# Kernel optimization log

Measured on AMD Instinct MI355X. Metric: run time of the kernel, lower is better.

Reference implementation:

```python
import jax, jax.numpy as jnp
import numpy as np

EPS = 1e-5

def _bn(x, gamma, beta):
    # training-mode BatchNorm1d over (batch, length) per channel; x: [B, C, N]
    mean = x.mean(axis=(0, 2), keepdims=True)
    var = x.var(axis=(0, 2), keepdims=True)
    return (x - mean) * jax.lax.rsqrt(var + EPS) * gamma[None, :, None] + beta[None, :, None]

def setup_inputs() -> dict:
    key = jax.random.key(0)
    ks = jax.random.split(key, 16)
    B, N = 8, 4096
    def w(k, o, i):
        return jax.random.normal(k, (o, i), jnp.float32) * (1.0 / np.sqrt(i))
    return {
        "x": jax.random.normal(ks[0], (B, 3, N), jnp.float32),
        "w_mlp1": w(ks[1], 64, 3),
        "g1": jax.random.uniform(ks[2], (64,), jnp.float32, 0.5, 1.5),
        "b1": jax.random.normal(ks[3], (64,), jnp.float32) * 0.1,
        "w_mlp2": w(ks[4], 128, 64),
        "wq": w(ks[5], 16, 128),
        "g2": jax.random.uniform(ks[6], (16,), jnp.float32, 0.5, 1.5),
        "b2": jax.random.normal(ks[7], (16,), jnp.float32) * 0.1,
        "wk": w(ks[8], 16, 128),
        "g3": jax.random.uniform(ks[9], (16,), jnp.float32, 0.5, 1.5),
        "b3": jax.random.normal(ks[10], (16,), jnp.float32) * 0.1,
        "wv": w(ks[11], 3, 128),
        "g4": jax.random.uniform(ks[12], (3,), jnp.float32, 0.5, 1.5),
        "b4": jax.random.normal(ks[13], (3,), jnp.float32) * 0.1,
        "alpha": jax.random.uniform(ks[14], (1,), jnp.float32, 0.1, 1.0),
    }

def reference(x, w_mlp1, g1, b1, w_mlp2, wq, g2, b2, wk, g3, b3, wv, g4, b4, alpha):
    # mlp: conv1(k=1) -> BN -> LeakyReLU(0.2) -> conv1(k=1)
    h = jnp.einsum('oc,bcn->bon', w_mlp1, x)                       # [B,64,N]
    h = jax.nn.leaky_relu(_bn(h, g1, b1), negative_slope=0.2)
    feat = jnp.einsum('oc,bcn->bon', w_mlp2, h)                    # [B,128,N]
    q = jax.nn.relu(_bn(jnp.einsum('oc,bcn->bon', wq, feat), g2, b2))  # [B,16,N]
    k = jax.nn.relu(_bn(jnp.einsum('oc,bcn->bon', wk, feat), g3, b3))  # [B,16,N]
    v = jax.nn.relu(_bn(jnp.einsum('oc,bcn->bon', wv, feat), g4, b4))  # [B,3,N]
    # similarity = softmax(K^T Q) over last dim (no scale, as in source)
    sim = jax.nn.softmax(jnp.einsum('bdn,bdm->bnm', k, q), axis=-1)    # [B,N,N]
    # out = V @ sim^T
    out = jnp.einsum('bcm,bnm->bcn', v, sim)                           # [B,3,N]
    return alpha[0] * out + x
```

## Files before the change

kernel.cpp:

```cpp
#include <hip/hip_runtime.h>

#define EPS 1e-5f
constexpr int NN = 4096;
constexpr float INV_CNT = 1.0f / (8.0f * 4096.0f);
constexpr float LOG2E = 1.44269504f;

typedef __attribute__((ext_vector_type(8))) short bf16x8;
typedef __attribute__((ext_vector_type(4))) float f32x4;
typedef __attribute__((ext_vector_type(16))) float f32x16;
typedef __attribute__((ext_vector_type(4))) _Float16 f16x4;
typedef __fp16 fp16x2 __attribute__((ext_vector_type(2)));

#if __has_builtin(__builtin_amdgcn_exp2f)
#define EXP2F(x) __builtin_amdgcn_exp2f(x)
#else
#define EXP2F(x) exp2f(x)
#endif

constexpr size_t OFF_QPT = 0;
constexpr size_t OFF_KPT = 524288;
constexpr size_t OFF_VPT = 1048576;
constexpr size_t OFF_WT2 = 1179648;
constexpr size_t OFF_XP  = 1181952;
constexpr size_t OFF_BS  = 1183104;
constexpr size_t OFF_QH  = 1201024;
constexpr size_t OFF_QL  = 1463168;
constexpr size_t OFF_KH  = 1725312;
constexpr size_t OFF_KL  = 1987456;
constexpr size_t OFF_VFH = 2249600;
constexpr size_t OFF_PL  = 2511744;
constexpr size_t OFF_PA0 = 2773888;
constexpr size_t OFF_PA1 = 3036032;
constexpr size_t OFF_PA2 = 3298176;
constexpr size_t OFF_PMX = 3560320;

__global__ __launch_bounds__(256) void kA_mom_wcomb(
    const float* __restrict__ x, float* __restrict__ xpart,
    const float* __restrict__ w2, const float* __restrict__ wq,
    const float* __restrict__ wk, const float* __restrict__ wv,
    float* __restrict__ wt2) {
  __shared__ float w2s[8192];
  __shared__ float wr[4480];
  __shared__ float sred[36];
  int tx = threadIdx.x;
  if (blockIdx.x < 128) {
    int idx = blockIdx.x * 256 + tx;
    int b = idx >> 12, n = idx & 4095;
    float x0 = x[(size_t)(b*3+0)*NN + n];
    float x1 = x[(size_t)(b*3+1)*NN + n];
    float x2 = x[(size_t)(b*3+2)*NN + n];
    float m[9] = {x0, x1, x2, x0*x0, x0*x1, x0*x2, x1*x1, x1*x2, x2*x2};
    #pragma unroll
    for (int off = 32; off; off >>= 1) {
      #pragma unroll
      for (int j = 0; j < 9; ++j) m[j] += __shfl_xor(m[j], off);
    }
    int w = tx >> 6;
    if ((tx & 63) == 0) {
      #pragma unroll
      for (int j = 0; j < 9; ++j) sred[w*9+j] = m[j];
    }
    __syncthreads();
    if (tx < 9) xpart[tx*128 + blockIdx.x] = sred[tx] + sred[9+tx] + sred[18+tx] + sred[27+tx];
  } else {
    for (int i = tx; i < 8192; i += 256) w2s[i] = w2[i];
    for (int i = tx; i < 2048; i += 256) { wr[i] = wq[i]; wr[2048+i] = wk[i]; }
    for (int i = tx; i < 384; i += 256) wr[4096+i] = wv[i];
    __syncthreads();
    for (int e = tx; e < 2240; e += 256) {
      int j = e >> 6, c = e & 63;
      float s = 0.f;
      #pragma unroll 4
      for (int o = 0; o < 128; ++o) s = fmaf(wr[j*128+o], w2s[o*64+c], s);
      wt2[c*36 + j] = s;
    }
  }
}

__global__ __launch_bounds__(128) void kB_qkv(
    const float* __restrict__ x, const float* __restrict__ xpart,
    const float* __restrict__ w1, const float* __restrict__ g1,
    const float* __restrict__ b1, const float* __restrict__ wt2,
    float* __restrict__ qpT, float* __restrict__ kpT, float* __restrict__ vpT,
    float* __restrict__ bs) {
  __shared__ float4 w1s[64];
  __shared__ float4 wt2s[576];
  __shared__ float sred[140];
  __shared__ float mom[9];
  int tx = threadIdx.x;
  for (int i = tx; i < 576; i += 128) wt2s[i] = ((const float4*)wt2)[i];
  if (tx < 9) {
    float acc = 0.f;
    #pragma unroll 8
    for (int i = 0; i < 128; ++i) acc += xpart[tx*128 + i];
    mom[tx] = acc * INV_CNT;
  }
  __syncthreads();
  if (tx < 64) {
    int c = tx;
    float a = w1[c*3], b_ = w1[c*3+1], d = w1[c*3+2];
    float mean = a*mom[0] + b_*mom[1] + d*mom[2];
    float e2 = a*a*mom[3] + b_*b_*mom[6] + d*d*mom[8]
             + 2.f*(a*b_*mom[4] + a*d*mom[5] + b_*d*mom[7]);
    float sc = g1[c] * rsqrtf(e2 - mean*mean + EPS);
    w1s[c] = make_float4(a*sc, b_*sc, d*sc, fmaf(-mean, sc, b1[c]));
  }
  __syncthreads();
  int idx = blockIdx.x*128 + tx;
  int b = idx >> 12, n = idx & 4095;
  float x0 = x[(size_t)(b*3+0)*NN + n];
  float x1 = x[(size_t)(b*3+1)*NN + n];
  float x2 = x[(size_t)(b*3+2)*NN + n];
  float qa[16] = {}, ka[16] = {};
  float va0 = 0.f, va1 = 0.f, va2 = 0.f;
  #pragma unroll 4
  for (int c = 0; c < 64; ++c) {
    float4 w = w1s[c];
    float h = fmaf(w.x, x0, fmaf(w.y, x1, fmaf(w.z, x2, w.w)));
    h = h > 0.f ? h : 0.2f*h;
    #pragma unroll
    for (int j = 0; j < 4; ++j) {
      float4 A = wt2s[c*9 + j];
      qa[4*j+0] = fmaf(A.x, h, qa[4*j+0]);
      qa[4*j+1] = fmaf(A.y, h, qa[4*j+1]);
      qa[4*j+2] = fmaf(A.z, h, qa[4*j+2]);
      qa[4*j+3] = fmaf(A.w, h, qa[4*j+3]);
      float4 B = wt2s[c*9 + 4 + j];
      ka[4*j+0] = fmaf(B.x, h, ka[4*j+0]);
      ka[4*j+1] = fmaf(B.y, h, ka[4*j+1]);
      ka[4*j+2] = fmaf(B.z, h, ka[4*j+2]);
      ka[4*j+3] = fmaf(B.w, h, ka[4*j+3]);
    }
    float4 V = wt2s[c*9 + 8];
    va0 = fmaf(V.x, h, va0); va1 = fmaf(V.y, h, va1); va2 = fmaf(V.z, h, va2);
  }
  float4* qo = (float4*)(qpT + (size_t)idx*16);
  float4* ko = (float4*)(kpT + (size_t)idx*16);
  #pragma unroll
  for (int j = 0; j < 4; ++j) {
    qo[j] = make_float4(qa[4*j], qa[4*j+1], qa[4*j+2], qa[4*j+3]);
    ko[j] = make_float4(ka[4*j], ka[4*j+1], ka[4*j+2], ka[4*j+3]);
  }
  ((float4*)vpT)[idx] = make_float4(va0, va1, va2, 0.f);
  int w = tx >> 6;
  bool lead = ((tx & 63) == 0);
  #pragma unroll
  for (int d = 0; d < 16; ++d) {
    float s = qa[d], q = qa[d]*qa[d];
    #pragma unroll
    for (int off = 32; off; off >>= 1) { s += __shfl_xor(s, off); q += __shfl_xor(q, off); }
    if (lead) { sred[w*70 + d] = s; sred[w*70 + 16 + d] = q; }
    s = ka[d]; q = ka[d]*ka[d];
    #pragma unroll
    for (int off = 32; off; off >>= 1) { s += __shfl_xor(s, off); q += __shfl_xor(q, off); }
    if (lead) { sred[w*70 + 32 + d] = s; sred[w*70 + 48 + d] = q; }
  }
  float vv[3] = {va0, va1, va2};
  #pragma unroll
  for (int d = 0; d < 3; ++d) {
    float s = vv[d], q = vv[d]*vv[d];
    #pragma unroll
    for (int off = 32; off; off >>= 1) { s += __shfl_xor(s, off); q += __shfl_xor(q, off); }
    if (lead) { sred[w*70 + 64 + d] = s; sred[w*70 + 67 + d] = q; }
  }
  __syncthreads();
  if (tx < 70)
    bs[tx*256 + blockIdx.x] = sred[tx] + sred[70+tx];
}

__global__ __launch_bounds__(256) void kC_prep(
    const float* __restrict__ qpT, const float* __restrict__ kpT,
    const float* __restrict__ vpT, const float* __restrict__ bs,
    const float* __restrict__ g2, const float* __restrict__ b2,
    const float* __restrict__ g3, const float* __restrict__ b3,
    const float* __restrict__ g4, const float* __restrict__ b4,
    uint4* __restrict__ qh, uint4* __restrict__ ql,
    uint4* __restrict__ kh, uint4* __restrict__ kl,
    _Float16* __restrict__ vfh) {
  __shared__ float tot[70];
  __shared__ float spr[70];
  int tx = threadIdx.x;
  if (tx < 70) {
    float acc = 0.f;
    #pragma unroll 8
    for (int i = 0; i < 256; ++i) acc += bs[tx*256 + i];
    tot[tx] = acc * INV_CNT;
  }
  __syncthreads();
  if (tx < 16) {
    float mean = tot[tx], var = tot[16+tx] - mean*mean;
    float sc = g2[tx]*rsqrtf(var + EPS);
    spr[tx] = sc * LOG2E;
    spr[16+tx] = fmaf(-mean, sc, b2[tx]) * LOG2E;
  } else if (tx < 32) {
    int d = tx-16;
    float mean = tot[32+d], var = tot[48+d] - mean*mean;
    float sc = g3[d]*rsqrtf(var + EPS);
    spr[32+d] = sc; spr[48+d] = fmaf(-mean, sc, b3[d]);
  } else if (tx < 35) {
    int d = tx-32;
    float mean = tot[64+d], var = tot[67+d] - mean*mean;
    float sc = g4[d]*rsqrtf(var + EPS);
    spr[64+d] = sc; spr[67+d] = fmaf(-mean, sc, b4[d]);
  }
  __syncthreads();
  int p = blockIdx.x*256 + tx;
  float qv[16], kv[16];
  const float4* q4 = (const float4*)(qpT + (size_t)p*16);
  const float4* k4p = (const float4*)(kpT + (size_t)p*16);
  #pragma unroll
  for (int j = 0; j < 4; ++j) {
    float4 tq = q4[j], tk = k4p[j];
    qv[4*j] = tq.x; qv[4*j+1] = tq.y; qv[4*j+2] = tq.z; qv[4*j+3] = tq.w;
    kv[4*j] = tk.x; kv[4*j+1] = tk.y; kv[4*j+2] = tk.z; kv[4*j+3] = tk.w;
  }
  #pragma unroll
  for (int d = 0; d < 16; ++d) {
    qv[d] = fmaxf(fmaf(qv[d], spr[d],    spr[16+d]), 0.f);
    kv[d] = fmaxf(fmaf(kv[d], spr[32+d], spr[48+d]), 0.f);
  }
  unsigned qhw[8], qlw[8], khw[8], klw[8];
  #pragma unroll
  for (int j = 0; j < 8; ++j) {
    unsigned u0 = __float_as_uint(qv[2*j]),   u1 = __float_as_uint(qv[2*j+1]);
    unsigned h0 = u0 & 0xFFFF0000u, h1 = u1 & 0xFFFF0000u;
    float l0 = qv[2*j] - __uint_as_float(h0);
    float l1 = qv[2*j+1] - __uint_as_float(h1);
    qhw[j] = (h0 >> 16) | h1;
    qlw[j] = (__float_as_uint(l0) >> 16) | (__float_as_uint(l1) & 0xFFFF0000u);
    u0 = __float_as_uint(kv[2*j]); u1 = __float_as_uint(kv[2*j+1]);
    h0 = u0 & 0xFFFF0000u; h1 = u1 & 0xFFFF0000u;
    l0 = kv[2*j] - __uint_as_float(h0);
    l1 = kv[2*j+1] - __uint_as_float(h1);
    khw[j] = (h0 >> 16) | h1;
    klw[j] = (__float_as_uint(l0) >> 16) | (__float_as_uint(l1) & 0xFFFF0000u);
  }
  qh[(size_t)p*2+0] = make_uint4(qhw[0], qhw[1], qhw[2], qhw[3]);
  qh[(size_t)p*2+1] = make_uint4(qhw[4], qhw[5], qhw[6], qhw[7]);
  ql[(size_t)p*2+0] = make_uint4(qlw[0], qlw[1], qlw[2], qlw[3]);
  ql[(size_t)p*2+1] = make_uint4(qlw[4], qlw[5], qlw[6], qlw[7]);
  kh[(size_t)p*2+0] = make_uint4(khw[0], khw[1], khw[2], khw[3]);
  kh[(size_t)p*2+1] = make_uint4(khw[4], khw[5], khw[6], khw[7]);
  kl[(size_t)p*2+0] = make_uint4(klw[0], klw[1], klw[2], klw[3]);
  kl[(size_t)p*2+1] = make_uint4(klw[4], klw[5], klw[6], klw[7]);
  float4 vv = ((const float4*)vpT)[p];
  vfh[0*32768 + p] = (_Float16)fmaxf(fmaf(vv.x, spr[64], spr[67]), 0.f);
  vfh[1*32768 + p] = (_Float16)fmaxf(fmaf(vv.y, spr[65], spr[68]), 0.f);
  vfh[2*32768 + p] = (_Float16)fmaxf(fmaf(vv.z, spr[66], spr[69]), 0.f);
  vfh[3*32768 + p] = (_Float16)1.0f;
}

__global__ __launch_bounds__(256, 4) void k5max(
    const uint4* __restrict__ qh, const uint4* __restrict__ kh,
    float* __restrict__ pmax2) {
  int tx = threadIdx.x;
  int cc = blockIdx.x & 3;
  int rc = (blockIdx.x >> 2) & 31;
  int b  = blockIdx.x >> 7;
  int w = tx >> 6, lane = tx & 63;
  int cl = lane & 31, hl = lane >> 5;
  int n0 = rc*128 + w*32;
  size_t pbase = (size_t)b*4096;
  bf16x8 aK = *(const bf16x8*)&kh[(pbase + n0 + cl)*2 + hl];
  f32x16 zero16;
  #pragma unroll
  for (int r = 0; r < 16; ++r) zero16[r] = 0.f;
  f32x16 lm = zero16;
  const uint4* qptr = &qh[(pbase + (size_t)cc*1024 + cl)*2 + hl];
  bf16x8 bQ1 = *(const bf16x8*)qptr;
  bf16x8 bQ2 = *(const bf16x8*)(qptr + 64);
  #pragma unroll 2
  for (int ct = 0; ct < 16; ++ct) {
    bf16x8 q1 = bQ1, q2 = bQ2;
    qptr += 128;
    if (ct < 15) {
      bQ1 = *(const bf16x8*)qptr;
      bQ2 = *(const bf16x8*)(qptr + 64);
    }
    f32x16 c1 = __builtin_amdgcn_mfma_f32_32x32x16_bf16(aK, q1, zero16, 0, 0, 0);
    f32x16 c2 = __builtin_amdgcn_mfma_f32_32x32x16_bf16(aK, q2, zero16, 0, 0, 0);
    #pragma unroll
    for (int r = 0; r < 16; ++r)
      lm[r] = fmaxf(fmaxf(lm[r], c1[r]), c2[r]);
  }
  #pragma unroll
  for (int off = 1; off <= 16; off <<= 1) {
    #pragma unroll
    for (int r = 0; r < 16; ++r) lm[r] = fmaxf(lm[r], __shfl_xor(lm[r], off));
  }
  if (cl == 0) {
    #pragma unroll
    for (int r = 0; r < 16; ++r)
      pmax2[(size_t)cc*32768 + pbase + n0 + (r & 3) + 8*(r >> 2) + 4*hl] = lm[r];
  }
}

#define K5_TILE(BKH, BKL, MR, ACC)                                             \
  {                                                                            \
    f32x4 c = __builtin_amdgcn_mfma_f32_16x16x32_bf16(aQ, BKH, zero4, 0, 0, 0);\
    c = __builtin_amdgcn_mfma_f32_16x16x32_bf16(aQ, BKL, c, 0, 0, 0);          \
    union { fp16x2 h2[2]; f16x4 v4; } pw;                                      \
    pw.h2[0] = __builtin_amdgcn_cvt_pkrtz(EXP2F(c[0] - MR), EXP2F(c[1] - MR)); \
    pw.h2[1] = __builtin_amdgcn_cvt_pkrtz(EXP2F(c[2] - MR), EXP2F(c[3] - MR)); \
    ACC = __builtin_amdgcn_mfma_f32_16x16x16f16(av, pw.v4, ACC, 0, 0, 0);      \
  }

__global__ __launch_bounds__(128, 5) void k5pv(
    const uint4* __restrict__ qh, const uint4* __restrict__ ql,
    const uint4* __restrict__ kh, const uint4* __restrict__ kl,
    const _Float16* __restrict__ vfh, const float* __restrict__ pmax2,
    float* __restrict__ pl, float* __restrict__ pa0,
    float* __restrict__ pa1, float* __restrict__ pa2) {
  int tx = threadIdx.x;
  int cb = blockIdx.x & 7;
  int rb = blockIdx.x >> 3;
  int b  = rb >> 5;
  int rc = rb & 31;
  int w = tx >> 6, lane = tx & 63;
  int nl = lane & 15, g = lane >> 4, g1 = g & 1;
  int n0 = rc*128 + w*64;
  size_t pbase = (size_t)b*4096;
  size_t kp0 = (pbase + n0 + nl)*2 + g1;
  bf16x8 bKh0 = *(const bf16x8*)&kh[kp0];
  bf16x8 bKl0 = *(const bf16x8*)&kl[kp0];
  bf16x8 bKh1 = *(const bf16x8*)&kh[kp0 + 32];
  bf16x8 bKl1 = *(const bf16x8*)&kl[kp0 + 32];
  bf16x8 bKh2 = *(const bf16x8*)&kh[kp0 + 64];
  bf16x8 bKl2 = *(const bf16x8*)&kl[kp0 + 64];
  bf16x8 bKh3 = *(const bf16x8*)&kh[kp0 + 96];
  bf16x8 bKl3 = *(const bf16x8*)&kl[kp0 + 96];
  size_t mi = pbase + n0 + nl;
  float M0, M1, M2, M3;
  {
    float a0 = fmaxf(pmax2[mi],      pmax2[32768 + mi]);
    float b0 = fmaxf(pmax2[2*32768 + mi], pmax2[3*32768 + mi]);
    M0 = fmaxf(a0, b0);
    a0 = fmaxf(pmax2[mi+16],      pmax2[32768 + mi+16]);
    b0 = fmaxf(pmax2[2*32768 + mi+16], pmax2[3*32768 + mi+16]);
    M1 = fmaxf(a0, b0);
    a0 = fmaxf(pmax2[mi+32],      pmax2[32768 + mi+32]);
    b0 = fmaxf(pmax2[2*32768 + mi+32], pmax2[3*32768 + mi+32]);
    M2 = fmaxf(a0, b0);
    a0 = fmaxf(pmax2[mi+48],      pmax2[32768 + mi+48]);
    b0 = fmaxf(pmax2[2*32768 + mi+48], pmax2[3*32768 + mi+48]);
    M3 = fmaxf(a0, b0);
  }
  f32x4 zero4 = {0.f, 0.f, 0.f, 0.f};
  f32x4 acc0 = zero4, acc1 = zero4, acc2 = zero4, acc3 = zero4;
  size_t cbase = pbase + (size_t)cb*512;
  const uint4* qptr = ((g < 2) ? qh : ql) + (cbase + nl)*2 + g1;
  const _Float16* vptr = vfh + (size_t)nl*32768 + cbase + g*4;
  bool vload = (nl < 4);
  f16x4 zeroh = {(_Float16)0.f, (_Float16)0.f, (_Float16)0.f, (_Float16)0.f};
  bf16x8 aQn = *(const bf16x8*)qptr;
  f16x4 avn = zeroh;
  if (vload) avn = *(const f16x4*)vptr;
  #pragma unroll 2
  for (int ct = 0; ct < 32; ++ct) {
    bf16x8 aQ = aQn;
    f16x4 av = avn;
    qptr += 32;
    vptr += 16;
    if (ct < 31) {
      aQn = *(const bf16x8*)qptr;
      if (vload) avn = *(const f16x4*)vptr;
    }
    K5_TILE(bKh0, bKl0, M0, acc0)
    K5_TILE(bKh1, bKl1, M1, acc1)
    K5_TILE(bKh2, bKl2, M2, acc2)
    K5_TILE(bKh3, bKl3, M3, acc3)
  }
  if (lane < 16) {
    size_t base = (size_t)cb*32768 + pbase + n0 + lane;
    pl[base]      = acc0[3]; pa0[base]      = acc0[0]; pa1[base]      = acc0[1]; pa2[base]      = acc0[2];
    pl[base + 16] = acc1[3]; pa0[base + 16] = acc1[0]; pa1[base + 16] = acc1[1]; pa2[base + 16] = acc1[2];
    pl[base + 32] = acc2[3]; pa0[base + 32] = acc2[0]; pa1[base + 32] = acc2[1]; pa2[base + 32] = acc2[2];
    pl[base + 48] = acc3[3]; pa0[base + 48] = acc3[0]; pa1[base + 48] = acc3[1]; pa2[base + 48] = acc3[2];
  }
}

__global__ __launch_bounds__(256) void k6_merge(
    const float* __restrict__ pl, const float* __restrict__ pa0,
    const float* __restrict__ pa1, const float* __restrict__ pa2,
    const float* __restrict__ x, const float* __restrict__ alpha,
    float* __restrict__ out) {
  int row = blockIdx.x*256 + threadIdx.x;
  float L = 0.f, A0 = 0.f, A1 = 0.f, A2 = 0.f;
  #pragma unroll
  for (int cb = 0; cb < 8; ++cb) {
    size_t i = (size_t)cb*32768 + row;
    L += pl[i]; A0 += pa0[i]; A1 += pa1[i]; A2 += pa2[i];
  }
  int b = row >> 12, n = row & 4095;
  float inv = 1.f / L, al = alpha[0];
  out[(size_t)(b*3+0)*NN + n] = fmaf(al, A0*inv, x[(size_t)(b*3+0)*NN + n]);
  out[(size_t)(b*3+1)*NN + n] = fmaf(al, A1*inv, x[(size_t)(b*3+1)*NN + n]);
  out[(size_t)(b*3+2)*NN + n] = fmaf(al, A2*inv, x[(size_t)(b*3+2)*NN + n]);
}

extern "C" void kernel_launch(void* const* d_in, const int* in_sizes, int n_in,
                              void* d_out, int out_size, void* d_ws, size_t ws_size,
                              hipStream_t stream) {
  const float* x    = (const float*)d_in[0];
  const float* w1   = (const float*)d_in[1];
  const float* g1   = (const float*)d_in[2];
  const float* b1   = (const float*)d_in[3];
  const float* w2   = (const float*)d_in[4];
  const float* wq   = (const float*)d_in[5];
  const float* g2   = (const float*)d_in[6];
  const float* b2   = (const float*)d_in[7];
  const float* wk   = (const float*)d_in[8];
  const float* g3   = (const float*)d_in[9];
  const float* b3   = (const float*)d_in[10];
  const float* wv   = (const float*)d_in[11];
  const float* g4   = (const float*)d_in[12];
  const float* b4   = (const float*)d_in[13];
  const float* alpha= (const float*)d_in[14];
  float* out = (float*)d_out;
  float* ws  = (float*)d_ws;

  float* qpT = ws + OFF_QPT;
  float* kpT = ws + OFF_KPT;
  float* vpT = ws + OFF_VPT;
  float* wt2 = ws + OFF_WT2;
  float* xp  = ws + OFF_XP;
  float* bst = ws + OFF_BS;
  uint4* qhb = (uint4*)(ws + OFF_QH);
  uint4* qlb = (uint4*)(ws + OFF_QL);
  uint4* khb = (uint4*)(ws + OFF_KH);
  uint4* klb = (uint4*)(ws + OFF_KL);
  _Float16* vfh = (_Float16*)(ws + OFF_VFH);
  float* pls = ws + OFF_PL;
  float* pa0 = ws + OFF_PA0;
  float* pa1 = ws + OFF_PA1;
  float* pa2 = ws + OFF_PA2;
  float* pmx = ws + OFF_PMX;

  kA_mom_wcomb<<<129, 256, 0, stream>>>(x, xp, w2, wq, wk, wv, wt2);
  kB_qkv<<<256, 128, 0, stream>>>(x, xp, w1, g1, b1, wt2, qpT, kpT, vpT, bst);
  kC_prep<<<128, 256, 0, stream>>>(qpT, kpT, vpT, bst, g2, b2, g3, b3, g4, b4,
                                   qhb, qlb, khb, klb, vfh);
  k5max<<<1024, 256, 0, stream>>>(qhb, khb, pmx);
  k5pv<<<2048, 128, 0, stream>>>(qhb, qlb, khb, klb, vfh, pmx, pls, pa0, pa1, pa2);
  k6_merge<<<128, 256, 0, stream>>>(pls, pa0, pa1, pa2, x, alpha, out);
}
```

Baseline: 94.32 us.

## Fuse row-max pass into PV kernel with per-chunk max and rescaled merge

Removes the separate k5max kernel that computed global row maxima over all columns. Each k5pv block now computes a local max over its own 512-column chunk in a bf16-high-only MFMA pre-pass, writes that max alongside its partial sums, and k6_merge rescales the partials by exp2 of the difference to the global max. This drops one kernel launch and a full extra scan of Q across the whole row, in exchange for a per-chunk pre-pass inside k5pv and one extra partial array to read in the merge. The local max starts at 0 and uses only the high bf16 part, so the subtracted max is approximate, which the exp2 rescaling tolerates.

```diff
diff --git a/kernel.cpp b/kernel.cpp
--- a/kernel.cpp
+++ b/kernel.cpp
@@ -7,7 +7,6 @@
 
 typedef __attribute__((ext_vector_type(8))) short bf16x8;
 typedef __attribute__((ext_vector_type(4))) float f32x4;
-typedef __attribute__((ext_vector_type(16))) float f32x16;
 typedef __attribute__((ext_vector_type(4))) _Float16 f16x4;
 typedef __fp16 fp16x2 __attribute__((ext_vector_type(2)));
 
@@ -32,7 +31,7 @@
 constexpr size_t OFF_PA0 = 2773888;
 constexpr size_t OFF_PA1 = 3036032;
 constexpr size_t OFF_PA2 = 3298176;
-constexpr size_t OFF_PMX = 3560320;
+constexpr size_t OFF_PM  = 3560320;
 
 __global__ __launch_bounds__(256) void kA_mom_wcomb(
     const float* __restrict__ x, float* __restrict__ xpart,
@@ -250,51 +249,6 @@
   vfh[3*32768 + p] = (_Float16)1.0f;
 }
 
-__global__ __launch_bounds__(256, 4) void k5max(
-    const uint4* __restrict__ qh, const uint4* __restrict__ kh,
-    float* __restrict__ pmax2) {
-  int tx = threadIdx.x;
-  int cc = blockIdx.x & 3;
-  int rc = (blockIdx.x >> 2) & 31;
-  int b  = blockIdx.x >> 7;
-  int w = tx >> 6, lane = tx & 63;
-  int cl = lane & 31, hl = lane >> 5;
-  int n0 = rc*128 + w*32;
-  size_t pbase = (size_t)b*4096;
-  bf16x8 aK = *(const bf16x8*)&kh[(pbase + n0 + cl)*2 + hl];
-  f32x16 zero16;
-  #pragma unroll
-  for (int r = 0; r < 16; ++r) zero16[r] = 0.f;
-  f32x16 lm = zero16;
-  const uint4* qptr = &qh[(pbase + (size_t)cc*1024 + cl)*2 + hl];
-  bf16x8 bQ1 = *(const bf16x8*)qptr;
-  bf16x8 bQ2 = *(const bf16x8*)(qptr + 64);
-  #pragma unroll 2
-  for (int ct = 0; ct < 16; ++ct) {
-    bf16x8 q1 = bQ1, q2 = bQ2;
-    qptr += 128;
-    if (ct < 15) {
-      bQ1 = *(const bf16x8*)qptr;
-      bQ2 = *(const bf16x8*)(qptr + 64);
-    }
-    f32x16 c1 = __builtin_amdgcn_mfma_f32_32x32x16_bf16(aK, q1, zero16, 0, 0, 0);
-    f32x16 c2 = __builtin_amdgcn_mfma_f32_32x32x16_bf16(aK, q2, zero16, 0, 0, 0);
-    #pragma unroll
-    for (int r = 0; r < 16; ++r)
-      lm[r] = fmaxf(fmaxf(lm[r], c1[r]), c2[r]);
-  }
-  #pragma unroll
-  for (int off = 1; off <= 16; off <<= 1) {
-    #pragma unroll
-    for (int r = 0; r < 16; ++r) lm[r] = fmaxf(lm[r], __shfl_xor(lm[r], off));
-  }
-  if (cl == 0) {
-    #pragma unroll
-    for (int r = 0; r < 16; ++r)
-      pmax2[(size_t)cc*32768 + pbase + n0 + (r & 3) + 8*(r >> 2) + 4*hl] = lm[r];
-  }
-}
-
 #define K5_TILE(BKH, BKL, MR, ACC)                                             \
   {                                                                            \
     f32x4 c = __builtin_amdgcn_mfma_f32_16x16x32_bf16(aQ, BKH, zero4, 0, 0, 0);\
@@ -308,8 +262,8 @@
 __global__ __launch_bounds__(128, 5) void k5pv(
     const uint4* __restrict__ qh, const uint4* __restrict__ ql,
     const uint4* __restrict__ kh, const uint4* __restrict__ kl,
-    const _Float16* __restrict__ vfh, const float* __restrict__ pmax2,
-    float* __restrict__ pl, float* __restrict__ pa0,
+    const _Float16* __restrict__ vfh,
+    float* __restrict__ pm, float* __restrict__ pl, float* __restrict__ pa0,
     float* __restrict__ pa1, float* __restrict__ pa2) {
   int tx = threadIdx.x;
   int cb = blockIdx.x & 7;
@@ -329,26 +283,34 @@
   bf16x8 bKl2 = *(const bf16x8*)&kl[kp0 + 64];
   bf16x8 bKh3 = *(const bf16x8*)&kh[kp0 + 96];
   bf16x8 bKl3 = *(const bf16x8*)&kl[kp0 + 96];
-  size_t mi = pbase + n0 + nl;
-  float M0, M1, M2, M3;
+  f32x4 zero4 = {0.f, 0.f, 0.f, 0.f};
+  size_t cbase = pbase + (size_t)cb*512;
+  const uint4* qbase = ((g < 2) ? qh : ql) + (cbase + nl)*2 + g1;
+  float M0 = 0.f, M1 = 0.f, M2 = 0.f, M3 = 0.f;
   {
-    float a0 = fmaxf(pmax2[mi],      pmax2[32768 + mi]);
-    float b0 = fmaxf(pmax2[2*32768 + mi], pmax2[3*32768 + mi]);
-    M0 = fmaxf(a0, b0);
-    a0 = fmaxf(pmax2[mi+16],      pmax2[32768 + mi+16]);
-    b0 = fmaxf(pmax2[2*32768 + mi+16], pmax2[3*32768 + mi+16]);
-    M1 = fmaxf(a0, b0);
-    a0 = fmaxf(pmax2[mi+32],      pmax2[32768 + mi+32]);
-    b0 = fmaxf(pmax2[2*32768 + mi+32], pmax2[3*32768 + mi+32]);
-    M2 = fmaxf(a0, b0);
-    a0 = fmaxf(pmax2[mi+48],      pmax2[32768 + mi+48]);
-    b0 = fmaxf(pmax2[2*32768 + mi+48], pmax2[3*32768 + mi+48]);
-    M3 = fmaxf(a0, b0);
-  }
-  f32x4 zero4 = {0.f, 0.f, 0.f, 0.f};
+    const uint4* qp2 = qbase;
+    bf16x8 aQn = *(const bf16x8*)qp2;
+    #pragma unroll 2
+    for (int ct = 0; ct < 32; ++ct) {
+      bf16x8 aQ = aQn;
+      qp2 += 32;
+      if (ct < 31) aQn = *(const bf16x8*)qp2;
+      f32x4 c0 = __builtin_amdgcn_mfma_f32_16x16x32_bf16(aQ, bKh0, zero4, 0, 0, 0);
+      f32x4 c1 = __builtin_amdgcn_mfma_f32_16x16x32_bf16(aQ, bKh1, zero4, 0, 0, 0);
+      f32x4 c2 = __builtin_amdgcn_mfma_f32_16x16x32_bf16(aQ, bKh2, zero4, 0, 0, 0);
+      f32x4 c3 = __builtin_amdgcn_mfma_f32_16x16x32_bf16(aQ, bKh3, zero4, 0, 0, 0);
+      M0 = fmaxf(fmaxf(fmaxf(M0, c0[0]), fmaxf(c0[1], c0[2])), c0[3]);
+      M1 = fmaxf(fmaxf(fmaxf(M1, c1[0]), fmaxf(c1[1], c1[2])), c1[3]);
+      M2 = fmaxf(fmaxf(fmaxf(M2, c2[0]), fmaxf(c2[1], c2[2])), c2[3]);
+      M3 = fmaxf(fmaxf(fmaxf(M3, c3[0]), fmaxf(c3[1], c3[2])), c3[3]);
+    }
+    M0 = fmaxf(M0, __shfl_xor(M0, 16)); M0 = fmaxf(M0, __shfl_xor(M0, 32));
+    M1 = fmaxf(M1, __shfl_xor(M1, 16)); M1 = fmaxf(M1, __shfl_xor(M1, 32));
+    M2 = fmaxf(M2, __shfl_xor(M2, 16)); M2 = fmaxf(M2, __shfl_xor(M2, 32));
+    M3 = fmaxf(M3, __shfl_xor(M3, 16)); M3 = fmaxf(M3, __shfl_xor(M3, 32));
+  }
   f32x4 acc0 = zero4, acc1 = zero4, acc2 = zero4, acc3 = zero4;
-  size_t cbase = pbase + (size_t)cb*512;
-  const uint4* qptr = ((g < 2) ? qh : ql) + (cbase + nl)*2 + g1;
+  const uint4* qptr = qbase;
   const _Float16* vptr = vfh + (size_t)nl*32768 + cbase + g*4;
   bool vload = (nl < 4);
   f16x4 zeroh = {(_Float16)0.f, (_Float16)0.f, (_Float16)0.f, (_Float16)0.f};
@@ -372,24 +334,33 @@
   }
   if (lane < 16) {
     size_t base = (size_t)cb*32768 + pbase + n0 + lane;
-    pl[base]      = acc0[3]; pa0[base]      = acc0[0]; pa1[base]      = acc0[1]; pa2[base]      = acc0[2];
-    pl[base + 16] = acc1[3]; pa0[base + 16] = acc1[0]; pa1[base + 16] = acc1[1]; pa2[base + 16] = acc1[2];
-    pl[base + 32] = acc2[3]; pa0[base + 32] = acc2[0]; pa1[base + 32] = acc2[1]; pa2[base + 32] = acc2[2];
-    pl[base + 48] = acc3[3]; pa0[base + 48] = acc3[0]; pa1[base + 48] = acc3[1]; pa2[base + 48] = acc3[2];
+    pm[base]      = M0; pl[base]      = acc0[3]; pa0[base]      = acc0[0]; pa1[base]      = acc0[1]; pa2[base]      = acc0[2];
+    pm[base + 16] = M1; pl[base + 16] = acc1[3]; pa0[base + 16] = acc1[0]; pa1[base + 16] = acc1[1]; pa2[base + 16] = acc1[2];
+    pm[base + 32] = M2; pl[base + 32] = acc2[3]; pa0[base + 32] = acc2[0]; pa1[base + 32] = acc2[1]; pa2[base + 32] = acc2[2];
+    pm[base + 48] = M3; pl[base + 48] = acc3[3]; pa0[base + 48] = acc3[0]; pa1[base + 48] = acc3[1]; pa2[base + 48] = acc3[2];
   }
 }
 
 __global__ __launch_bounds__(256) void k6_merge(
-    const float* __restrict__ pl, const float* __restrict__ pa0,
-    const float* __restrict__ pa1, const float* __restrict__ pa2,
-    const float* __restrict__ x, const float* __restrict__ alpha,
-    float* __restrict__ out) {
+    const float* __restrict__ pm, const float* __restrict__ pl,
+    const float* __restrict__ pa0, const float* __restrict__ pa1,
+    const float* __restrict__ pa2, const float* __restrict__ x,
+    const float* __restrict__ alpha, float* __restrict__ out) {
   int row = blockIdx.x*256 + threadIdx.x;
+  float m[8];
+  #pragma unroll
+  for (int cb = 0; cb < 8; ++cb) m[cb] = pm[(size_t)cb*32768 + row];
+  float M = fmaxf(fmaxf(fmaxf(m[0], m[1]), fmaxf(m[2], m[3])),
+                  fmaxf(fmaxf(m[4], m[5]), fmaxf(m[6], m[7])));
   float L = 0.f, A0 = 0.f, A1 = 0.f, A2 = 0.f;
   #pragma unroll
   for (int cb = 0; cb < 8; ++cb) {
     size_t i = (size_t)cb*32768 + row;
-    L += pl[i]; A0 += pa0[i]; A1 += pa1[i]; A2 += pa2[i];
+    float ci = EXP2F(m[cb] - M);
+    L  = fmaf(pl[i],  ci, L);
+    A0 = fmaf(pa0[i], ci, A0);
+    A1 = fmaf(pa1[i], ci, A1);
+    A2 = fmaf(pa2[i], ci, A2);
   }
   int b = row >> 12, n = row & 4095;
   float inv = 1.f / L, al = alpha[0];
@@ -434,13 +405,12 @@
   float* pa0 = ws + OFF_PA0;
   float* pa1 = ws + OFF_PA1;
   float* pa2 = ws + OFF_PA2;
-  float* pmx = ws + OFF_PMX;
+  float* pms = ws + OFF_PM;
 
   kA_mom_wcomb<<<129, 256, 0, stream>>>(x, xp, w2, wq, wk, wv, wt2);
   kB_qkv<<<256, 128, 0, stream>>>(x, xp, w1, g1, b1, wt2, qpT, kpT, vpT, bst);
   kC_prep<<<128, 256, 0, stream>>>(qpT, kpT, vpT, bst, g2, b2, g3, b3, g4, b4,
                                    qhb, qlb, khb, klb, vfh);
-  k5max<<<1024, 256, 0, stream>>>(qhb, khb, pmx);
-  k5pv<<<2048, 128, 0, stream>>>(qhb, qlb, khb, klb, vfh, pmx, pls, pa0, pa1, pa2);
-  k6_merge<<<128, 256, 0, stream>>>(pls, pa0, pa1, pa2, x, alpha, out);
-}
+  k5pv<<<2048, 128, 0, stream>>>(qhb, qlb, khb, klb, vfh, pms, pls, pa0, pa1, pa2);
+  k6_merge<<<128, 256, 0, stream>>>(pms, pls, pa0, pa1, pa2, x, alpha, out);
+}
```

Result: no change. 92.95 us (median of 2 runs) (-1.5%).
